# Optimization experiments

Hardware: AMD Instinct MI355X
Metric: run time of the kernel (lower is better)

The kernel has to match this reference:

```python
import jax, jax.numpy as jnp
import numpy as np

HIDDEN = 2048
NUM_HEADS = 8
NUM_KV_HEADS = 1
HEAD_DIM = 256
ROPE_THETA = 10000.0
T = 2048  # num tokens (single causal prefill sequence)
Q_SIZE = NUM_HEADS * HEAD_DIM        # 2048
KV_SIZE = NUM_KV_HEADS * HEAD_DIM    # 256


def _apply_rope(x, positions):
    # x: [T, n_heads, head_dim], neox style (rotate halves)
    half = HEAD_DIM // 2
    inv_freq = 1.0 / (ROPE_THETA ** (jnp.arange(half, dtype=jnp.float32) * 2.0 / HEAD_DIM))
    ang = positions.astype(jnp.float32)[:, None] * inv_freq[None, :]   # [T, half]
    cos = jnp.cos(ang)[:, None, :]
    sin = jnp.sin(ang)[:, None, :]
    x1, x2 = jnp.split(x, 2, axis=-1)
    return jnp.concatenate([x1 * cos - x2 * sin, x2 * cos + x1 * sin], axis=-1)


def setup_inputs() -> dict:
    key = jax.random.key(0)
    k1, k2, k3 = jax.random.split(key, 3)
    hidden_states = jax.random.normal(k1, (T, HIDDEN), dtype=jnp.float32)
    Wqkv = jax.random.normal(k2, (Q_SIZE + 2 * KV_SIZE, HIDDEN), dtype=jnp.float32) * 0.02
    Wo = jax.random.normal(k3, (HIDDEN, Q_SIZE), dtype=jnp.float32) * 0.02
    positions = jnp.arange(T, dtype=jnp.int32)
    return {"positions": positions, "hidden_states": hidden_states, "Wqkv": Wqkv, "Wo": Wo}


def reference(positions, hidden_states, Wqkv, Wo):
    scaling = HEAD_DIM ** -0.5
    qkv = hidden_states @ Wqkv.T                                   # [T, Q+2KV]
    q = qkv[:, :Q_SIZE].reshape(T, NUM_HEADS, HEAD_DIM)
    k = qkv[:, Q_SIZE:Q_SIZE + KV_SIZE].reshape(T, NUM_KV_HEADS, HEAD_DIM)
    v = qkv[:, Q_SIZE + KV_SIZE:].reshape(T, NUM_KV_HEADS, HEAD_DIM)
    q = _apply_rope(q, positions)
    k = _apply_rope(k, positions)
    # GQA: group query heads over kv heads
    g = NUM_HEADS // NUM_KV_HEADS
    qg = q.reshape(T, NUM_KV_HEADS, g, HEAD_DIM)
    scores = jnp.einsum('qhgd,khd->hgqk', qg, k) * scaling         # [kv, g, T, T]
    causal = jnp.arange(T)[:, None] >= jnp.arange(T)[None, :]
    scores = jnp.where(causal[None, None], scores, jnp.finfo(scores.dtype).min)
    probs = jax.nn.softmax(scores, axis=-1)
    attn = jnp.einsum('hgqk,khd->qhgd', probs, v).reshape(T, Q_SIZE)
    return attn @ Wo.T
```

## Files before the change

kernel.cpp:

```cpp
#include <hip/hip_runtime.h>
#include <hip/hip_bf16.h>

typedef __bf16 bf16x8 __attribute__((ext_vector_type(8)));
typedef __bf16 bf16x4 __attribute__((ext_vector_type(4)));
typedef float floatx4 __attribute__((ext_vector_type(4)));

__device__ __forceinline__ float fast_exp2(float x) {
    return __builtin_amdgcn_exp2f(x);
}

__device__ __forceinline__ void lds_barrier() {
    asm volatile("s_waitcnt lgkmcnt(0)\n\ts_barrier" ::: "memory");
}

__device__ __forceinline__ void gload16(const __bf16* g, __bf16* l) {
    __builtin_amdgcn_global_load_lds((const __attribute__((address_space(1))) void*)g,
                                     (__attribute__((address_space(3))) void*)l, 16, 0, 0);
}

__global__ __launch_bounds__(256) void cast_all(const float* __restrict__ hid,
                                                const float* __restrict__ wqkv,
                                                const float* __restrict__ wo,
                                                __bf16* __restrict__ Ah,
                                                __bf16* __restrict__ Wqkvh,
                                                __bf16* __restrict__ Woh) {
    const int n1 = 1048576, n2 = 1310720;
    int i = blockIdx.x * 256 + threadIdx.x;
    const float* in;
    __bf16* out;
    int j;
    if (i < n1) { in = hid; out = Ah; j = i; }
    else if (i < n1 + n2) { in = wqkv; out = Wqkvh; j = i - n1; }
    else { in = wo; out = Woh; j = i - n1 - n2; }
    float4 v = ((const float4*)in)[j];
    bf16x4 o;
    o[0] = (__bf16)v.x; o[1] = (__bf16)v.y; o[2] = (__bf16)v.z; o[3] = (__bf16)v.w;
    ((bf16x4*)out)[j] = o;
}

__global__ __launch_bounds__(256) void gemm_bt_splitk(const __bf16* __restrict__ A,
                                                      const __bf16* __restrict__ B,
                                                      __bf16* __restrict__ C,
                                                      int M, int N, int K) {
    __shared__ __attribute__((aligned(16))) __bf16 As[128 * 64];
    __shared__ __attribute__((aligned(16))) __bf16 Bs[128 * 64];

    int tid = threadIdx.x, lane = tid & 63, w = tid >> 6;
    int wm = (w >> 1) * 64, wn = (w & 1) * 64;
    int bm0 = blockIdx.x * 128, bn0 = blockIdx.y * 128;
    int r = lane & 15, q4 = lane >> 4;
    int rr = lane >> 2, qq = lane & 3;
    int Khalf = K >> 1;
    int kbase = (int)blockIdx.z * Khalf;

    const __bf16* Agp[4];
    const __bf16* Bgp[4];
    __bf16* Asd[4];
    __bf16* Bsd[4];
#pragma unroll
    for (int j = 0; j < 4; j++) {
        int c = w * 4 + j;
        int kk = c >> 3, g = c & 7;
        Agp[j] = A + (size_t)(bm0 + g * 16 + rr) * K + kbase + kk * 32 + qq * 8;
        Bgp[j] = B + (size_t)(bn0 + g * 16 + rr) * K + kbase + kk * 32 + qq * 8;
        Asd[j] = &As[c * 512];
        Bsd[j] = &Bs[c * 512];
    }

    floatx4 acc[4][4];
#pragma unroll
    for (int i = 0; i < 4; i++)
#pragma unroll
        for (int j = 0; j < 4; j++) acc[i][j] = (floatx4)0.f;

    for (int k0 = 0; k0 < Khalf; k0 += 64) {
        asm volatile("s_barrier" ::: "memory");
#pragma unroll
        for (int j = 0; j < 4; j++) {
            gload16(Agp[j] + k0, Asd[j]);
            gload16(Bgp[j] + k0, Bsd[j]);
        }
        asm volatile("s_waitcnt vmcnt(0)\n\ts_barrier" ::: "memory");

#pragma unroll
        for (int kk = 0; kk < 2; kk++) {
            bf16x8 a[4], b[4];
#pragma unroll
            for (int mt = 0; mt < 4; mt++)
                a[mt] = *(const bf16x8*)&As[(kk * 8 + (wm >> 4) + mt) * 512 + r * 32 + q4 * 8];
#pragma unroll
            for (int nt = 0; nt < 4; nt++)
                b[nt] = *(const bf16x8*)&Bs[(kk * 8 + (wn >> 4) + nt) * 512 + r * 32 + q4 * 8];
#pragma unroll
            for (int mt = 0; mt < 4; mt++)
#pragma unroll
                for (int nt = 0; nt < 4; nt++)
                    acc[mt][nt] = __builtin_amdgcn_mfma_f32_16x16x32_bf16(a[mt], b[nt], acc[mt][nt], 0, 0, 0);
        }
    }

    __bf16* Cp = C + (size_t)blockIdx.z * M * N;
#pragma unroll
    for (int mt = 0; mt < 4; mt++)
#pragma unroll
        for (int nt = 0; nt < 4; nt++) {
            int row = bm0 + wm + mt * 16 + q4 * 4;
            int col = bn0 + wn + nt * 16 + r;
#pragma unroll
            for (int i = 0; i < 4; i++)
                Cp[(size_t)(row + i) * N + col] = (__bf16)acc[mt][nt][i];
        }
}

__global__ __launch_bounds__(256) void rope_vtrans(const __bf16* __restrict__ qa,
                                                   const __bf16* __restrict__ qb,
                                                   const int* __restrict__ positions,
                                                   __bf16* __restrict__ Qo,
                                                   __bf16* __restrict__ Ko,
                                                   __bf16* __restrict__ Vt) {
    __shared__ float tile[32][33];
    int b = blockIdx.x;
    if (b < 9216) {
        int idx = b * 256 + threadIdx.x;
        int i = idx & 127;
        int th = idx >> 7;
        int head = th % 9;
        int t = th / 9;
        float invf = expf(-(float)i * 0.07195578415606394f);
        float ang = (float)positions[t] * invf;
        float s = sinf(ang), c = cosf(ang);
        size_t off = (size_t)t * 2560 + (head < 8 ? head * 256 : 2048);
        float x1 = (float)qa[off + i] + (float)qb[off + i];
        float x2 = (float)qa[off + i + 128] + (float)qb[off + i + 128];
        if (head < 8) {
            const float qs = 0.09016844f;
            __bf16* dst = Qo + (size_t)t * 2048 + head * 256;
            dst[i]       = (__bf16)((x1 * c - x2 * s) * qs);
            dst[i + 128] = (__bf16)((x2 * c + x1 * s) * qs);
        } else {
            int sw = (t & 7) << 3;
            __bf16* dst = Ko + (size_t)t * 256;
            dst[i ^ sw]         = (__bf16)(x1 * c - x2 * s);
            dst[(i + 128) ^ sw] = (__bf16)(x2 * c + x1 * s);
        }
    } else {
        int bb = b - 9216;
        int bt = bb & 63;
        int bc = bb >> 6;
        int tx = threadIdx.x & 31;
        int ty0 = threadIdx.x >> 5;
#pragma unroll
        for (int ty = ty0; ty < 32; ty += 8) {
            size_t gi = (size_t)(bt * 32 + ty) * 2560 + 2304 + bc * 32 + tx;
            tile[ty][tx] = (float)qa[gi] + (float)qb[gi];
        }
        __syncthreads();
#pragma unroll
        for (int ty = ty0; ty < 32; ty += 8)
            Vt[(size_t)bt * 8192 + (bc * 2 + (ty >> 4)) * 512 + (ty & 15) * 8
               + (tx >> 3) * 128 + (tx & 7)] = (__bf16)tile[tx][ty];
    }
}

__global__ __launch_bounds__(256, 2) void attn_kernel(const __bf16* __restrict__ Q,
                                                      const __bf16* __restrict__ Kg,
                                                      const __bf16* __restrict__ Vt,
                                                      __bf16* __restrict__ Opart,
                                                      float2* __restrict__ Ml) {
    __shared__ __attribute__((aligned(16))) __bf16 Ks[2][32 * 256];
    __shared__ __attribute__((aligned(16))) __bf16 Vs[2][16 * 512];
    __shared__ __attribute__((aligned(16))) __bf16 Ps[4][32][40];

    int hg = blockIdx.x;
    int rs = 203 - (int)blockIdx.y;
    int k, base;
    if (rs < 12)       { k = 1; base = 0; }
    else if (rs < 36)  { k = 2; base = 12; }
    else if (rs < 72)  { k = 3; base = 36; }
    else if (rs < 120) { k = 4; base = 72; }
    else if (rs < 180) { k = 5; base = 120; }
    else               { k = 6; base = 180; }
    int idx = rs - base;
    int s = idx % k;
    int g = (k - 1) * 12 + idx / k;
    int slot = base + idx - s;

    int start = s * 384;
    int end = g * 32 + 32;
    if (end > start + 384) end = start + 384;
    int ntiles = (end - start) >> 5;

    int tid = threadIdx.x, lane = tid & 63, w = tid >> 6;
    int r = lane & 15, q4 = lane >> 4;
    int h = hg * 4 + w;
    int sw = (r & 7) << 3;

    bf16x8 qf[2][8];
#pragma unroll
    for (int qt = 0; qt < 2; qt++) {
        const __bf16* qrow = Q + (size_t)(g * 32 + qt * 16 + r) * 2048 + h * 256 + q4 * 8;
#pragma unroll
        for (int ks = 0; ks < 8; ks++) qf[qt][ks] = *(const bf16x8*)(qrow + ks * 32);
    }

    bf16x8 ones;
#pragma unroll
    for (int i = 0; i < 8; i++) ones[i] = (__bf16)1.0f;

    floatx4 acc[2][16];
#pragma unroll
    for (int qt = 0; qt < 2; qt++)
#pragma unroll
        for (int i = 0; i < 16; i++) acc[qt][i] = (floatx4)0.f;
    floatx4 acc_l[2];
    acc_l[0] = (floatx4)0.f; acc_l[1] = (floatx4)0.f;

    {
        const __bf16* kp = Kg + (size_t)start * 256 + tid * 8;
        const __bf16* vp = Vt + (size_t)(start >> 5) * 8192 + tid * 8;
        __bf16* kl = &Ks[0][tid * 8];
        __bf16* vl = &Vs[0][tid * 8];
#pragma unroll
        for (int j = 0; j < 4; j++) {
            gload16(kp + j * 2048, kl + j * 2048);
            gload16(vp + j * 2048, vl + j * 2048);
        }
    }

    for (int t = 0; t < ntiles; t++) {
        int cb = t & 1;
        int kt0 = start + t * 32;
        asm volatile("s_barrier" ::: "memory");
        if (t + 1 < ntiles) {
            int kt1 = kt0 + 32;
            const __bf16* kp = Kg + (size_t)kt1 * 256 + tid * 8;
            const __bf16* vp = Vt + (size_t)(kt1 >> 5) * 8192 + tid * 8;
            __bf16* kl = &Ks[cb ^ 1][tid * 8];
            __bf16* vl = &Vs[cb ^ 1][tid * 8];
#pragma unroll
            for (int j = 0; j < 4; j++) {
                gload16(kp + j * 2048, kl + j * 2048);
                gload16(vp + j * 2048, vl + j * 2048);
            }
            asm volatile("s_waitcnt vmcnt(8)\n\ts_barrier" ::: "memory");
        } else {
            asm volatile("s_waitcnt vmcnt(0)\n\ts_barrier" ::: "memory");
        }

        floatx4 sc[2][2];
        sc[0][0] = (floatx4)0.f; sc[0][1] = (floatx4)0.f;
        sc[1][0] = (floatx4)0.f; sc[1][1] = (floatx4)0.f;
#pragma unroll
        for (int ks = 0; ks < 8; ks++) {
#pragma unroll
            for (int nt = 0; nt < 2; nt++) {
                bf16x8 kf = *(const bf16x8*)&Ks[cb][(nt * 16 + r) * 256 + ((ks * 32 + q4 * 8) ^ sw)];
#pragma unroll
                for (int qt = 0; qt < 2; qt++)
                    sc[qt][nt] = __builtin_amdgcn_mfma_f32_16x16x32_bf16(qf[qt][ks], kf, sc[qt][nt], 0, 0, 0);
            }
        }
        if (kt0 + 31 > g * 32) {
#pragma unroll
            for (int qt = 0; qt < 2; qt++) {
                int qbase = g * 32 + qt * 16 + q4 * 4;
#pragma unroll
                for (int nt = 0; nt < 2; nt++) {
                    int kpos = kt0 + nt * 16 + r;
#pragma unroll
                    for (int i = 0; i < 4; i++)
                        if (kpos > qbase + i) sc[qt][nt][i] = -3e38f;
                }
            }
        }

#pragma unroll
        for (int qt = 0; qt < 2; qt++)
#pragma unroll
            for (int nt = 0; nt < 2; nt++)
#pragma unroll
                for (int i = 0; i < 4; i++)
                    Ps[w][qt * 16 + q4 * 4 + i][(nt * 16 + r) ^ (q4 << 3)] = (__bf16)fast_exp2(sc[qt][nt][i]);
        __builtin_amdgcn_wave_barrier();
        bf16x8 pf[2];
#pragma unroll
        for (int qt = 0; qt < 2; qt++)
            pf[qt] = *(const bf16x8*)&Ps[w][qt * 16 + r][(q4 * 8) ^ ((r >> 2) << 3)];
        __builtin_amdgcn_wave_barrier();

#pragma unroll
        for (int n16 = 0; n16 < 16; n16++) {
            bf16x8 vf = *(const bf16x8*)&Vs[cb][n16 * 512 + lane * 8];
            acc[0][n16] = __builtin_amdgcn_mfma_f32_16x16x32_bf16(pf[0], vf, acc[0][n16], 0, 0, 0);
            acc[1][n16] = __builtin_amdgcn_mfma_f32_16x16x32_bf16(pf[1], vf, acc[1][n16], 0, 0, 0);
        }
        acc_l[0] = __builtin_amdgcn_mfma_f32_16x16x32_bf16(pf[0], ones, acc_l[0], 0, 0, 0);
        acc_l[1] = __builtin_amdgcn_mfma_f32_16x16x32_bf16(pf[1], ones, acc_l[1], 0, 0, 0);
    }

    size_t base_row = (size_t)(slot + s) * 256 + hg * 128 + w * 32;
#pragma unroll
    for (int qt = 0; qt < 2; qt++)
#pragma unroll
        for (int n16 = 0; n16 < 16; n16++)
#pragma unroll
            for (int i = 0; i < 4; i++)
                Opart[(base_row + qt * 16 + q4 * 4 + i) * 256 + n16 * 16 + r] = (__bf16)acc[qt][n16][i];
    if (r == 0) {
#pragma unroll
        for (int qt = 0; qt < 2; qt++)
#pragma unroll
            for (int i = 0; i < 4; i++)
                Ml[base_row + qt * 16 + q4 * 4 + i] = make_float2(0.f, acc_l[qt][i]);
    }
}

__global__ __launch_bounds__(256) void combine_kernel(const __bf16* __restrict__ Opart,
                                                      const float2* __restrict__ Ml,
                                                      __bf16* __restrict__ attnb) {
    int wid = blockIdx.x * 4 + (threadIdx.x >> 6);
    int lane = threadIdx.x & 63;
    int t = wid >> 3, h = wid & 7;
    int g = t >> 5, r32 = t & 31;
    int qt = r32 >> 4, row16 = r32 & 15;
    int hg = h >> 2, w = h & 3;
    int k = g / 12 + 1;
    int fg = 6 * k * (k - 1) + (g - 12 * (k - 1)) * k;

    float ls[6];
    size_t rbase[6];
    for (int s = 0; s < k; s++) {
        rbase[s] = (size_t)(fg + s) * 256 + hg * 128 + w * 32 + qt * 16 + row16;
        ls[s] = Ml[rbase[s]].y;
    }
    float L = 0.f;
    float o[4] = {0.f, 0.f, 0.f, 0.f};
    for (int s = 0; s < k; s++) {
        L += ls[s];
        bf16x4 v = *(const bf16x4*)&Opart[rbase[s] * 256 + lane * 4];
#pragma unroll
        for (int j = 0; j < 4; j++) o[j] += (float)v[j];
    }
    float inv = 1.f / L;
    bf16x4 ov;
#pragma unroll
    for (int j = 0; j < 4; j++) ov[j] = (__bf16)(o[j] * inv);
    *(bf16x4*)&attnb[(size_t)t * 2048 + h * 256 + lane * 4] = ov;
}

__global__ __launch_bounds__(256) void add_out(const __bf16* __restrict__ p0,
                                               const __bf16* __restrict__ p1,
                                               float* __restrict__ out, int n4) {
    int i = blockIdx.x * 256 + threadIdx.x;
    if (i < n4) {
        bf16x4 a = ((const bf16x4*)p0)[i];
        bf16x4 b = ((const bf16x4*)p1)[i];
        float4 o;
        o.x = (float)a[0] + (float)b[0];
        o.y = (float)a[1] + (float)b[1];
        o.z = (float)a[2] + (float)b[2];
        o.w = (float)a[3] + (float)b[3];
        ((float4*)out)[i] = o;
    }
}

extern "C" void kernel_launch(void* const* d_in, const int* in_sizes, int n_in,
                              void* d_out, int out_size, void* d_ws, size_t ws_size,
                              hipStream_t stream) {
    const int* positions = (const int*)d_in[0];
    const float* hidden  = (const float*)d_in[1];
    const float* Wqkv    = (const float*)d_in[2];
    const float* Wo      = (const float*)d_in[3];
    float* out = (float*)d_out;

    char* ws = (char*)d_ws;
    const size_t MB = 1024 * 1024;
    __bf16* Ah    = (__bf16*)(ws + 0 * MB);
    __bf16* Woh   = (__bf16*)(ws + 8 * MB);
    __bf16* Qb    = (__bf16*)(ws + 16 * MB);
    __bf16* Kb    = (__bf16*)(ws + 24 * MB);
    __bf16* Vtb   = (__bf16*)(ws + 25 * MB);
    __bf16* Wqkvh = (__bf16*)(ws + 26 * MB);
    __bf16* qkvp  = (__bf16*)(ws + 36 * MB);
    __bf16* qkv_a = qkvp;
    __bf16* qkv_b = qkvp + (size_t)2048 * 2560;
    __bf16* Opart = (__bf16*)(ws + 26 * MB);
    float2* Ml    = (float2*)(ws + 52 * MB);
    __bf16* attnb = Ah;
    __bf16* gp    = (__bf16*)(ws + 26 * MB);

    cast_all<<<13312, 256, 0, stream>>>(hidden, Wqkv, Wo, Ah, Wqkvh, Woh);

    gemm_bt_splitk<<<dim3(16, 20, 2), 256, 0, stream>>>(Ah, Wqkvh, qkvp, 2048, 2560, 2048);

    rope_vtrans<<<9728, 256, 0, stream>>>(qkv_a, qkv_b, positions, Qb, Kb, Vtb);

    attn_kernel<<<dim3(2, 204), 256, 0, stream>>>(Qb, Kb, Vtb, Opart, Ml);
    combine_kernel<<<4096, 256, 0, stream>>>(Opart, Ml, attnb);

    gemm_bt_splitk<<<dim3(16, 16, 2), 256, 0, stream>>>(attnb, Woh, gp, 2048, 2048, 2048);
    add_out<<<4096, 256, 0, stream>>>(gp, gp + (size_t)2048 * 2048, out, 1048576);
}
```

Measured before the change: 213.0 us.

## Double-buffer LDS tiles in split-K GEMM to overlap loads with MFMA

Allocates two LDS buffers for the A and B tiles and prefetches the next K-slice while computing on the current one. A partial vmcnt wait replaces the full drain, so global-to-LDS latency is hidden behind MFMA work. This doubles the GEMM's shared-memory footprint, which may reduce blocks per CU.

```diff
diff --git a/kernel.cpp b/kernel.cpp
--- a/kernel.cpp
+++ b/kernel.cpp
@@ -42,8 +42,8 @@
                                                       const __bf16* __restrict__ B,
                                                       __bf16* __restrict__ C,
                                                       int M, int N, int K) {
-    __shared__ __attribute__((aligned(16))) __bf16 As[128 * 64];
-    __shared__ __attribute__((aligned(16))) __bf16 Bs[128 * 64];
+    __shared__ __attribute__((aligned(16))) __bf16 As[2][128 * 64];
+    __shared__ __attribute__((aligned(16))) __bf16 Bs[2][128 * 64];
 
     int tid = threadIdx.x, lane = tid & 63, w = tid >> 6;
     int wm = (w >> 1) * 64, wn = (w & 1) * 64;
@@ -55,16 +55,14 @@
 
     const __bf16* Agp[4];
     const __bf16* Bgp[4];
-    __bf16* Asd[4];
-    __bf16* Bsd[4];
+    int coff[4];
 #pragma unroll
     for (int j = 0; j < 4; j++) {
         int c = w * 4 + j;
         int kk = c >> 3, g = c & 7;
         Agp[j] = A + (size_t)(bm0 + g * 16 + rr) * K + kbase + kk * 32 + qq * 8;
         Bgp[j] = B + (size_t)(bn0 + g * 16 + rr) * K + kbase + kk * 32 + qq * 8;
-        Asd[j] = &As[c * 512];
-        Bsd[j] = &Bs[c * 512];
+        coff[j] = c * 512;
     }
 
     floatx4 acc[4][4];
@@ -73,24 +71,38 @@
 #pragma unroll
         for (int j = 0; j < 4; j++) acc[i][j] = (floatx4)0.f;
 
-    for (int k0 = 0; k0 < Khalf; k0 += 64) {
+    int niter = Khalf >> 6;
+
+#pragma unroll
+    for (int j = 0; j < 4; j++) {
+        gload16(Agp[j], &As[0][coff[j]]);
+        gload16(Bgp[j], &Bs[0][coff[j]]);
+    }
+
+    for (int t = 0; t < niter; t++) {
+        int cb = t & 1;
+        int k0 = t << 6;
         asm volatile("s_barrier" ::: "memory");
-#pragma unroll
-        for (int j = 0; j < 4; j++) {
-            gload16(Agp[j] + k0, Asd[j]);
-            gload16(Bgp[j] + k0, Bsd[j]);
-        }
-        asm volatile("s_waitcnt vmcnt(0)\n\ts_barrier" ::: "memory");
+        if (t + 1 < niter) {
+#pragma unroll
+            for (int j = 0; j < 4; j++) {
+                gload16(Agp[j] + k0 + 64, &As[cb ^ 1][coff[j]]);
+                gload16(Bgp[j] + k0 + 64, &Bs[cb ^ 1][coff[j]]);
+            }
+            asm volatile("s_waitcnt vmcnt(8)\n\ts_barrier" ::: "memory");
+        } else {
+            asm volatile("s_waitcnt vmcnt(0)\n\ts_barrier" ::: "memory");
+        }
 
 #pragma unroll
         for (int kk = 0; kk < 2; kk++) {
             bf16x8 a[4], b[4];
 #pragma unroll
             for (int mt = 0; mt < 4; mt++)
-                a[mt] = *(const bf16x8*)&As[(kk * 8 + (wm >> 4) + mt) * 512 + r * 32 + q4 * 8];
+                a[mt] = *(const bf16x8*)&As[cb][(kk * 8 + (wm >> 4) + mt) * 512 + r * 32 + q4 * 8];
 #pragma unroll
             for (int nt = 0; nt < 4; nt++)
-                b[nt] = *(const bf16x8*)&Bs[(kk * 8 + (wn >> 4) + nt) * 512 + r * 32 + q4 * 8];
+                b[nt] = *(const bf16x8*)&Bs[cb][(kk * 8 + (wn >> 4) + nt) * 512 + r * 32 + q4 * 8];
 #pragma unroll
             for (int mt = 0; mt < 4; mt++)
 #pragma unroll
```

After: 218.2 us. +2.5%, slower.
